# Kernel tuning notes

Hardware: AMD Instinct MI355X
Metric: run time of the kernel (lower is better)

The kernel has to match this reference:

```python
import jax, jax.numpy as jnp
import numpy as np

N, E = 50000, 800000
IN, H, C = 256, 8, 32  # heads=8, hidden_dim=32 -> out dim 256
NEG_SLOPE = 0.2
EPS = 1e-5


def setup_inputs() -> dict:
    key = jax.random.key(0)
    ks = jax.random.split(key, 6)
    x = jax.random.normal(ks[0], (N, IN), jnp.float32)
    edge_index = jax.random.randint(ks[1], (2, E), 0, N, dtype=jnp.int32)
    W = jax.random.normal(ks[2], (IN, H * C), jnp.float32) / np.sqrt(IN).astype(np.float32)
    att_src = jax.random.normal(ks[3], (H, C), jnp.float32) * 0.1
    att_dst = jax.random.normal(ks[4], (H, C), jnp.float32) * 0.1
    bias = jnp.zeros((H * C,), jnp.float32)
    gamma = jnp.ones((H * C,), jnp.float32)
    beta = jnp.zeros((H * C,), jnp.float32)
    return {"x": x, "edge_index": edge_index, "W": W, "att_src": att_src,
            "att_dst": att_dst, "bias": bias, "gamma": gamma, "beta": beta}


def reference(x, edge_index, W, att_src, att_dst, bias, gamma, beta):
    n = x.shape[0]
    # Linear projection -> per-head features [N, H, C]
    xl = (x @ W).reshape(n, H, C)
    # Per-node attention half-logits [N, H]
    a_src = jnp.einsum('nhc,hc->nh', xl, att_src)
    a_dst = jnp.einsum('nhc,hc->nh', xl, att_dst)
    # Add self loops (PyG GATConv default)
    loops = jnp.arange(n, dtype=edge_index.dtype)
    src = jnp.concatenate([edge_index[0], loops])  # [E+N]
    dst = jnp.concatenate([edge_index[1], loops])
    # Edge attention logits + segment softmax over destination neighborhoods
    logits = jax.nn.leaky_relu(a_src[src] + a_dst[dst], NEG_SLOPE)  # [E+N, H]
    seg_max = jax.ops.segment_max(logits, dst, num_segments=n)
    ex = jnp.exp(logits - seg_max[dst])
    denom = jax.ops.segment_sum(ex, dst, num_segments=n)
    alpha = ex / denom[dst]  # [E+N, H]
    # Weighted scatter-aggregation of source features
    msgs = xl[src] * alpha[:, :, None]  # [E+N, H, C]
    out = jax.ops.segment_sum(msgs, dst, num_segments=n).reshape(n, H * C) + bias
    # LayerNorm over feature dim
    mu = jnp.mean(out, axis=-1, keepdims=True)
    var = jnp.var(out, axis=-1, keepdims=True)
    return (out - mu) / jnp.sqrt(var + EPS) * gamma + beta
```

## Files before the change

### kernel.cpp

```cpp
#include <hip/hip_runtime.h>
#include <math.h>

#define NEG 0.2f
#define LNEPS 1e-5f

typedef __attribute__((ext_vector_type(8))) short bf16x8;
typedef __attribute__((ext_vector_type(8))) unsigned short u16x8;
typedef __attribute__((ext_vector_type(4))) float f32x4;
typedef __attribute__((ext_vector_type(4))) unsigned int u32x4;

__device__ __forceinline__ float lrelu(float x){ return x > 0.f ? x : NEG*x; }

__device__ __forceinline__ short f2b(float f){
  unsigned u = __float_as_uint(f);
  unsigned r = u + 0x7fffu + ((u >> 16) & 1u);
  return (short)(r >> 16);
}
__device__ __forceinline__ float b2f(unsigned short u){
  return __uint_as_float(((unsigned)u) << 16);
}
__device__ __forceinline__ unsigned cvtpk(float lo, float hi){
  unsigned r;
  asm("v_cvt_pk_bf16_f32 %0, %1, %2" : "=v"(r) : "v"(lo), "v"(hi));
  return r;
}

__global__ __launch_bounds__(256) void wt_k(const float* __restrict__ W,
                                            const float* __restrict__ att_src,
                                            const float* __restrict__ att_dst,
                                            unsigned short* __restrict__ WT,
                                            unsigned short* __restrict__ WS,
                                            int* __restrict__ deg, int N){
  int b = blockIdx.x;
  if (b < 256){
    int idx = b*256 + threadIdx.x;
    int k = idx >> 8, c = idx & 255;
    WT[c*256 + k] = (unsigned short)f2b(W[idx]);
  } else if (b < 272){
    int idx = (b-256)*256 + threadIdx.x;
    int col = idx >> 8;
    int k   = idx & 255;
    int head = col & 7;
    const float* av = (col < 8 ? att_src : att_dst) + head*32;
    const float* wr = W + (size_t)k*256 + head*32;
    float sum = 0.f;
    #pragma unroll
    for (int c=0;c<32;c++) sum += wr[c]*av[c];
    WS[col*256 + k] = (unsigned short)f2b(sum);
  } else {
    int i = (b-272)*256 + threadIdx.x;
    if (i < N) deg[i] = 1;
  }
}

__device__ __forceinline__ void load_half(float4 nx[8], const float* p){
  #pragma unroll
  for (int s=0;s<4;s++){
    nx[2*s]   = *(const float4*)(p + s*32);
    nx[2*s+1] = *(const float4*)(p + s*32 + 4);
  }
}
__device__ __forceinline__ void cvt_half(bf16x8 af[4], const float4 nx[8]){
  #pragma unroll
  for (int s=0;s<4;s++){
    u32x4 q;
    q.x = cvtpk(nx[2*s].x,   nx[2*s].y);
    q.y = cvtpk(nx[2*s].z,   nx[2*s].w);
    q.z = cvtpk(nx[2*s+1].x, nx[2*s+1].y);
    q.w = cvtpk(nx[2*s+1].z, nx[2*s+1].w);
    af[s] = __builtin_bit_cast(bf16x8, q);
  }
}

__global__ __launch_bounds__(256, 2) void mfma_gemm_k(const float* __restrict__ A,
    const unsigned short* __restrict__ WT, const unsigned short* __restrict__ WS,
    unsigned short* __restrict__ Cb,
    float* __restrict__ a_src, float* __restrict__ a_dst, int M, int nTiles){
  int w   = threadIdx.x >> 6;
  int l   = threadIdx.x & 63;
  int l15 = l & 15;
  int kg  = l >> 4;
  int colbase = w*64;

  bf16x8 bfr[4][8];
  #pragma unroll
  for (int j=0;j<4;j++){
    const unsigned short* bp = WT + (size_t)(colbase + j*16 + l15)*256 + kg*8;
    #pragma unroll
    for (int ks=0;ks<8;ks++) bfr[j][ks] = *(const bf16x8*)(bp + ks*32);
  }
  bf16x8 bfa[8];
  if (w==0){
    const unsigned short* bp = WS + (size_t)l15*256 + kg*8;
    #pragma unroll
    for (int ks=0;ks<8;ks++) bfa[ks] = *(const bf16x8*)(bp + ks*32);
  }

  int t = blockIdx.x;
  if (t >= nTiles) return;
  int row0 = t*16 + l15;
  const float* ap = A + (size_t)(row0 < M ? row0 : M-1)*256 + kg*8;
  float4 nx[8];
  load_half(nx, ap);

  while (t < nTiles){
    f32x4 acc[4];
    #pragma unroll
    for (int j=0;j<4;j++) acc[j] = (f32x4){0.f,0.f,0.f,0.f};
    f32x4 acc_a = (f32x4){0.f,0.f,0.f,0.f};
    bf16x8 af[4];

    cvt_half(af, nx);
    load_half(nx, ap + 128);
    #pragma unroll
    for (int s=0;s<4;s++){
      #pragma unroll
      for (int j=0;j<4;j++)
        acc[j] = __builtin_amdgcn_mfma_f32_16x16x32_bf16(af[s], bfr[j][s], acc[j], 0, 0, 0);
      if (w==0)
        acc_a = __builtin_amdgcn_mfma_f32_16x16x32_bf16(af[s], bfa[s], acc_a, 0, 0, 0);
    }

    int tn = t + gridDim.x;
    int rown = tn < nTiles ? tn*16 + l15 : row0;
    const float* apn = A + (size_t)(rown < M ? rown : M-1)*256 + kg*8;

    cvt_half(af, nx);
    load_half(nx, apn);
    #pragma unroll
    for (int s=0;s<4;s++){
      #pragma unroll
      for (int j=0;j<4;j++)
        acc[j] = __builtin_amdgcn_mfma_f32_16x16x32_bf16(af[s], bfr[j][4+s], acc[j], 0, 0, 0);
      if (w==0)
        acc_a = __builtin_amdgcn_mfma_f32_16x16x32_bf16(af[s], bfa[4+s], acc_a, 0, 0, 0);
    }

    int orow_base = t*16 + kg*4;
    #pragma unroll
    for (int j=0;j<4;j++){
      #pragma unroll
      for (int rp=0;rp<2;rp++){
        unsigned pk = cvtpk(acc[j][2*rp], acc[j][2*rp+1]);
        int orow = orow_base + 2*rp;
        if (orow < M)   Cb[(size_t)orow*256     + colbase + j*16 + l15] = (unsigned short)(pk & 0xffffu);
        if (orow+1 < M) Cb[(size_t)(orow+1)*256 + colbase + j*16 + l15] = (unsigned short)(pk >> 16);
      }
    }
    if (w==0){
      #pragma unroll
      for (int rr=0;rr<4;rr++){
        int orow = orow_base + rr;
        if (orow < M){
          if (l15 < 8) a_src[(size_t)orow*8 + l15]     = acc_a[rr];
          else         a_dst[(size_t)orow*8 + l15 - 8] = acc_a[rr];
        }
      }
    }
    t = tn; row0 = rown; ap = apn;
  }
}

__global__ void deg_k(const int* __restrict__ dst, int* __restrict__ deg, int E){
  int e = blockIdx.x*blockDim.x+threadIdx.x;
  if (e<E) atomicAdd(&deg[dst[e]],1);
}

__global__ __launch_bounds__(1024) void scan1_k(const int* __restrict__ deg,
                                                int* __restrict__ off,
                                                int* __restrict__ bsum, int n){
  __shared__ int wsum[16];
  int tid=threadIdx.x, lane=tid&63, wid=tid>>6;
  int i = blockIdx.x*1024 + tid;
  int v = (i<n)?deg[i]:0;
  int x = v;
  #pragma unroll
  for (int s=1;s<64;s<<=1){ int t2=__shfl_up(x,s); if (lane>=s) x+=t2; }
  if (lane==63) wsum[wid]=x;
  __syncthreads();
  if (tid<16){
    int y=wsum[tid];
    #pragma unroll
    for (int s=1;s<16;s<<=1){ int t2=__shfl_up(y,s); if (tid>=s) y+=t2; }
    wsum[tid]=y;
  }
  __syncthreads();
  int prefix=(wid? wsum[wid-1]:0);
  if (i<n) off[i]=prefix + x - v;
  if (tid==0) bsum[blockIdx.x]=wsum[15];
}

__global__ void scan2_k(int* __restrict__ bsum, int nb, int* __restrict__ offn){
  int lane = threadIdx.x;
  int v = (lane<nb)?bsum[lane]:0;
  int x = v;
  #pragma unroll
  for (int s=1;s<64;s<<=1){ int t2=__shfl_up(x,s); if (lane>=s) x+=t2; }
  if (lane<nb) bsum[lane] = x - v;
  if (lane==63) *offn = x;
}

__global__ __launch_bounds__(1024) void scan3self_k(int* __restrict__ off,
    const int* __restrict__ bsum, int* __restrict__ sorted, int* __restrict__ cur, int n){
  int i = blockIdx.x*1024 + threadIdx.x;
  if (i>=n) return;
  int o = off[i] + bsum[blockIdx.x];
  off[i] = o;
  sorted[o] = i;
  cur[i] = 1;
}

__global__ void scatter_k(const int* __restrict__ src, const int* __restrict__ dst,
                          const int* __restrict__ off, int* __restrict__ cur,
                          int* __restrict__ sorted, int E){
  int e=blockIdx.x*blockDim.x+threadIdx.x;
  if (e<E){
    int d=dst[e];
    int pos=off[d]+atomicAdd(&cur[d],1);
    sorted[pos]=src[e];
  }
}

__global__ __launch_bounds__(256) void agg5_k(const unsigned short* __restrict__ xlb,
    const float* __restrict__ a_src, const float* __restrict__ a_dst,
    const int* __restrict__ off, const int* __restrict__ sorted,
    const float* __restrict__ bias, const float* __restrict__ gamma,
    const float* __restrict__ beta, float* __restrict__ out, int n){
  int node = blockIdx.x*4 + (threadIdx.x>>6);
  if (node >= n) return;
  int lane = threadIdx.x & 63;
  int half = lane >> 5;
  int sl   = lane & 31;
  int h    = sl >> 2;
  int hh   = lane & 7;
  int je   = lane >> 3;
  float adst_h = a_dst[(size_t)node*8 + h];
  float adst_e = a_dst[(size_t)node*8 + hh];
  int s0 = off[node], dd = off[node+1] - s0;

  float acc[8] = {0.f,0.f,0.f,0.f,0.f,0.f,0.f,0.f};
  float den = 0.f;

  int i = 0;
  for (; i+8 <= dd; i += 8){
    int s[4];
    #pragma unroll
    for (int j=0;j<4;j++) s[j] = sorted[s0 + i + 2*j + half];
    int se = sorted[s0 + i + je];
    float w_l = __expf(lrelu(a_src[(size_t)se*8 + hh] + adst_e));
    float wv[4];
    #pragma unroll
    for (int j=0;j<4;j++) wv[j] = __shfl(w_l, ((2*j+half)<<3) | h);
    u16x8 u[4];
    #pragma unroll
    for (int j=0;j<4;j++) u[j] = *(const u16x8*)(xlb + (size_t)s[j]*256 + sl*8);
    #pragma unroll
    for (int j=0;j<4;j++){
      den += wv[j];
      #pragma unroll
      for (int k=0;k<8;k++) acc[k] += wv[j]*b2f((unsigned short)u[j][k]);
    }
  }
  for (; i < dd; i += 2){
    int idx = i + half;
    bool ok = idx < dd;
    int s1 = ok ? sorted[s0+idx] : node;
    float w1 = ok ? __expf(lrelu(a_src[(size_t)s1*8+h]+adst_h)) : 0.f;
    u16x8 u1 = *(const u16x8*)(xlb + (size_t)s1*256 + sl*8);
    den += w1;
    #pragma unroll
    for (int k=0;k<8;k++) acc[k] += w1*b2f((unsigned short)u1[k]);
  }

  den += __shfl_xor(den, 32);
  #pragma unroll
  for (int k=0;k<8;k++) acc[k] += __shfl_xor(acc[k], 32);

  float rd = 1.0f/den;
  float4 bia0 = *(const float4*)(bias + sl*8);
  float4 bia1 = *(const float4*)(bias + sl*8 + 4);
  float o[8];
  o[0]=acc[0]*rd+bia0.x; o[1]=acc[1]*rd+bia0.y; o[2]=acc[2]*rd+bia0.z; o[3]=acc[3]*rd+bia0.w;
  o[4]=acc[4]*rd+bia1.x; o[5]=acc[5]*rd+bia1.y; o[6]=acc[6]*rd+bia1.z; o[7]=acc[7]*rd+bia1.w;

  float sum=0.f, ssq=0.f;
  #pragma unroll
  for (int k=0;k<8;k++){ sum += o[k]; ssq += o[k]*o[k]; }
  #pragma unroll
  for (int s=1;s<32;s<<=1){ sum += __shfl_xor(sum,s); ssq += __shfl_xor(ssq,s); }
  float mean = sum*(1.0f/256.0f);
  float var  = ssq*(1.0f/256.0f) - mean*mean;
  float rstd = rsqrtf(var + LNEPS);

  int f = sl*8 + half*4;
  float4 g  = *(const float4*)(gamma + f);
  float4 be = *(const float4*)(beta + f);
  int kb = half*4;
  float4 ov;
  ov.x = (o[kb+0]-mean)*rstd*g.x+be.x;
  ov.y = (o[kb+1]-mean)*rstd*g.y+be.y;
  ov.z = (o[kb+2]-mean)*rstd*g.z+be.z;
  ov.w = (o[kb+3]-mean)*rstd*g.w+be.w;
  *(float4*)(out + (size_t)node*256 + f) = ov;
}

extern "C" void kernel_launch(void* const* d_in, const int* in_sizes, int n_in,
                              void* d_out, int out_size, void* d_ws, size_t ws_size,
                              hipStream_t stream){
  const float* x       = (const float*)d_in[0];
  const int*   ei      = (const int*)  d_in[1];
  const float* W       = (const float*)d_in[2];
  const float* att_src = (const float*)d_in[3];
  const float* att_dst = (const float*)d_in[4];
  const float* bias    = (const float*)d_in[5];
  const float* gamma   = (const float*)d_in[6];
  const float* beta    = (const float*)d_in[7];
  float* out = (float*)d_out;

  int N = in_sizes[0]/256;
  int E = in_sizes[1]/2;
  const int* srcp = ei;
  const int* dstp = ei + E;

  unsigned short* xlb = (unsigned short*)d_ws;
  float* a_src = (float*)(xlb + (size_t)N*256);
  float* a_dst = a_src + (size_t)N*8;
  int*   deg   = (int*)(a_dst + (size_t)N*8);
  int*   off   = deg + N;
  int*   cur   = off + N + 1;
  int*   sorted= cur + N;
  int*   bsum  = sorted + E + N;
  unsigned short* WT = (unsigned short*)(bsum + 1024);
  unsigned short* WS = WT + 65536;

  int nb = (N + 1023)/1024;
  int nbI = (N + 255)/256;
  int nTiles = (N + 15)/16;

  wt_k<<<272 + nbI, 256, 0, stream>>>(W, att_src, att_dst, WT, WS, deg, N);
  mfma_gemm_k<<<512, 256, 0, stream>>>(x, WT, WS, xlb, a_src, a_dst, N, nTiles);
  deg_k<<<(E+255)/256, 256, 0, stream>>>(dstp, deg, E);
  scan1_k<<<nb, 1024, 0, stream>>>(deg, off, bsum, N);
  scan2_k<<<1, 64, 0, stream>>>(bsum, nb, off + N);
  scan3self_k<<<nb, 1024, 0, stream>>>(off, bsum, sorted, cur, N);
  scatter_k<<<(E+255)/256, 256, 0, stream>>>(srcp, dstp, off, cur, sorted, E);
  agg5_k<<<(N+3)/4, 256, 0, stream>>>(xlb, a_src, a_dst, off, sorted, bias, gamma, beta, out, N);
}
```

Baseline: 210.8 us.

## Stage GEMM A tile through swizzled LDS and merge degree/scan launches

```diff
diff --git a/kernel.cpp b/kernel.cpp
--- a/kernel.cpp
+++ b/kernel.cpp
@@ -28,9 +28,10 @@
 __global__ __launch_bounds__(256) void wt_k(const float* __restrict__ W,
                                             const float* __restrict__ att_src,
                                             const float* __restrict__ att_dst,
+                                            const int* __restrict__ dst,
                                             unsigned short* __restrict__ WT,
                                             unsigned short* __restrict__ WS,
-                                            int* __restrict__ deg, int N){
+                                            int* __restrict__ deg, int E){
   int b = blockIdx.x;
   if (b < 256){
     int idx = b*256 + threadIdx.x;
@@ -45,30 +46,24 @@
     const float* wr = W + (size_t)k*256 + head*32;
     float sum = 0.f;
     #pragma unroll
-    for (int c=0;c<32;c++) sum += wr[c]*av[c];
+    for (int c2=0;c2<32;c2++) sum += wr[c2]*av[c2];
     WS[col*256 + k] = (unsigned short)f2b(sum);
   } else {
-    int i = (b-272)*256 + threadIdx.x;
-    if (i < N) deg[i] = 1;
-  }
-}
-
-__device__ __forceinline__ void load_half(float4 nx[8], const float* p){
-  #pragma unroll
-  for (int s=0;s<4;s++){
-    nx[2*s]   = *(const float4*)(p + s*32);
-    nx[2*s+1] = *(const float4*)(p + s*32 + 4);
-  }
-}
-__device__ __forceinline__ void cvt_half(bf16x8 af[4], const float4 nx[8]){
-  #pragma unroll
-  for (int s=0;s<4;s++){
-    u32x4 q;
-    q.x = cvtpk(nx[2*s].x,   nx[2*s].y);
-    q.y = cvtpk(nx[2*s].z,   nx[2*s].w);
-    q.z = cvtpk(nx[2*s+1].x, nx[2*s+1].y);
-    q.w = cvtpk(nx[2*s+1].z, nx[2*s+1].w);
-    af[s] = __builtin_bit_cast(bf16x8, q);
+    int e = (b-272)*256 + threadIdx.x;
+    if (e < E) atomicAdd(&deg[dst[e]], 1);
+  }
+}
+
+__device__ __forceinline__ void load_tile(float4 v[4], const float* __restrict__ A,
+                                          int t, int M, int tid){
+  const float* base = A + (size_t)t*4096;
+  int rmax = M - 1 - t*16;
+  #pragma unroll
+  for (int j=0;j<4;j++){
+    int idx4 = (j>>1)*512 + 2*tid + (j&1);
+    int r = idx4 >> 6;
+    if (r > rmax) idx4 = (rmax<<6) | (idx4 & 63);
+    v[j] = *(const float4*)(base + (size_t)idx4*4);
   }
 }
 
@@ -76,8 +71,10 @@
     const unsigned short* __restrict__ WT, const unsigned short* __restrict__ WS,
     unsigned short* __restrict__ Cb,
     float* __restrict__ a_src, float* __restrict__ a_dst, int M, int nTiles){
-  int w   = threadIdx.x >> 6;
-  int l   = threadIdx.x & 63;
+  __shared__ __align__(16) unsigned short Asb[16*256];
+  int tid = threadIdx.x;
+  int w   = tid >> 6;
+  int l   = tid & 63;
   int l15 = l & 15;
   int kg  = l >> 4;
   int colbase = w*64;
@@ -98,42 +95,42 @@
 
   int t = blockIdx.x;
   if (t >= nTiles) return;
-  int row0 = t*16 + l15;
-  const float* ap = A + (size_t)(row0 < M ? row0 : M-1)*256 + kg*8;
-  float4 nx[8];
-  load_half(nx, ap);
+  float4 v[4];
+  load_tile(v, A, t, M, tid);
 
   while (t < nTiles){
+    __syncthreads();
+    #pragma unroll
+    for (int p=0;p<2;p++){
+      u32x4 q;
+      q.x = cvtpk(v[2*p].x,   v[2*p].y);
+      q.y = cvtpk(v[2*p].z,   v[2*p].w);
+      q.z = cvtpk(v[2*p+1].x, v[2*p+1].y);
+      q.w = cvtpk(v[2*p+1].z, v[2*p+1].w);
+      int slot = p*256 + tid;
+      int sw = slot ^ ((slot>>5)&7);
+      *(u32x4*)(Asb + (size_t)sw*8) = q;
+    }
+    __syncthreads();
+
+    int tn = t + gridDim.x;
+    if (tn < nTiles) load_tile(v, A, tn, M, tid);
+
     f32x4 acc[4];
     #pragma unroll
     for (int j=0;j<4;j++) acc[j] = (f32x4){0.f,0.f,0.f,0.f};
     f32x4 acc_a = (f32x4){0.f,0.f,0.f,0.f};
-    bf16x8 af[4];
-
-    cvt_half(af, nx);
-    load_half(nx, ap + 128);
-    #pragma unroll
-    for (int s=0;s<4;s++){
+
+    #pragma unroll
+    for (int s=0;s<8;s++){
+      int slot = l15*32 + kg + s*4;
+      int sw = slot ^ (l15 & 7);
+      bf16x8 af = *(const bf16x8*)(Asb + (size_t)sw*8);
       #pragma unroll
       for (int j=0;j<4;j++)
-        acc[j] = __builtin_amdgcn_mfma_f32_16x16x32_bf16(af[s], bfr[j][s], acc[j], 0, 0, 0);
+        acc[j] = __builtin_amdgcn_mfma_f32_16x16x32_bf16(af, bfr[j][s], acc[j], 0, 0, 0);
       if (w==0)
-        acc_a = __builtin_amdgcn_mfma_f32_16x16x32_bf16(af[s], bfa[s], acc_a, 0, 0, 0);
-    }
-
-    int tn = t + gridDim.x;
-    int rown = tn < nTiles ? tn*16 + l15 : row0;
-    const float* apn = A + (size_t)(rown < M ? rown : M-1)*256 + kg*8;
-
-    cvt_half(af, nx);
-    load_half(nx, apn);
-    #pragma unroll
-    for (int s=0;s<4;s++){
-      #pragma unroll
-      for (int j=0;j<4;j++)
-        acc[j] = __builtin_amdgcn_mfma_f32_16x16x32_bf16(af[s], bfr[j][4+s], acc[j], 0, 0, 0);
-      if (w==0)
-        acc_a = __builtin_amdgcn_mfma_f32_16x16x32_bf16(af[s], bfa[4+s], acc_a, 0, 0, 0);
+        acc_a = __builtin_amdgcn_mfma_f32_16x16x32_bf16(af, bfa[s], acc_a, 0, 0, 0);
     }
 
     int orow_base = t*16 + kg*4;
@@ -157,13 +154,8 @@
         }
       }
     }
-    t = tn; row0 = rown; ap = apn;
-  }
-}
-
-__global__ void deg_k(const int* __restrict__ dst, int* __restrict__ deg, int E){
-  int e = blockIdx.x*blockDim.x+threadIdx.x;
-  if (e<E) atomicAdd(&deg[dst[e]],1);
+    t = tn;
+  }
 }
 
 __global__ __launch_bounds__(1024) void scan1_k(const int* __restrict__ deg,
@@ -172,7 +164,7 @@
   __shared__ int wsum[16];
   int tid=threadIdx.x, lane=tid&63, wid=tid>>6;
   int i = blockIdx.x*1024 + tid;
-  int v = (i<n)?deg[i]:0;
+  int v = (i<n)?(deg[i]+1):0;
   int x = v;
   #pragma unroll
   for (int s=1;s<64;s<<=1){ int t2=__shfl_up(x,s); if (lane>=s) x+=t2; }
@@ -190,21 +182,21 @@
   if (tid==0) bsum[blockIdx.x]=wsum[15];
 }
 
-__global__ void scan2_k(int* __restrict__ bsum, int nb, int* __restrict__ offn){
-  int lane = threadIdx.x;
-  int v = (lane<nb)?bsum[lane]:0;
-  int x = v;
-  #pragma unroll
-  for (int s=1;s<64;s<<=1){ int t2=__shfl_up(x,s); if (lane>=s) x+=t2; }
-  if (lane<nb) bsum[lane] = x - v;
-  if (lane==63) *offn = x;
-}
-
 __global__ __launch_bounds__(1024) void scan3self_k(int* __restrict__ off,
-    const int* __restrict__ bsum, int* __restrict__ sorted, int* __restrict__ cur, int n){
+    const int* __restrict__ bsum, int* __restrict__ sorted, int* __restrict__ cur,
+    int n, int total){
+  __shared__ int prefs;
+  if (threadIdx.x < 64){
+    int v = ((int)threadIdx.x < blockIdx.x) ? bsum[threadIdx.x] : 0;
+    #pragma unroll
+    for (int s=1;s<64;s<<=1) v += __shfl_xor(v, s);
+    if (threadIdx.x==0) prefs = v;
+  }
+  __syncthreads();
   int i = blockIdx.x*1024 + threadIdx.x;
+  if (blockIdx.x==0 && threadIdx.x==0) off[n] = total;
   if (i>=n) return;
-  int o = off[i] + bsum[blockIdx.x];
+  int o = off[i] + prefs;
   off[i] = o;
   sorted[o] = i;
   cur[i] = 1;
@@ -334,15 +326,13 @@
   unsigned short* WS = WT + 65536;
 
   int nb = (N + 1023)/1024;
-  int nbI = (N + 255)/256;
   int nTiles = (N + 15)/16;
 
-  wt_k<<<272 + nbI, 256, 0, stream>>>(W, att_src, att_dst, WT, WS, deg, N);
+  hipMemsetAsync(deg, 0, (size_t)N*sizeof(int), stream);
+  wt_k<<<272 + (E+255)/256, 256, 0, stream>>>(W, att_src, att_dst, dstp, WT, WS, deg, E);
   mfma_gemm_k<<<512, 256, 0, stream>>>(x, WT, WS, xlb, a_src, a_dst, N, nTiles);
-  deg_k<<<(E+255)/256, 256, 0, stream>>>(dstp, deg, E);
   scan1_k<<<nb, 1024, 0, stream>>>(deg, off, bsum, N);
-  scan2_k<<<1, 64, 0, stream>>>(bsum, nb, off + N);
-  scan3self_k<<<nb, 1024, 0, stream>>>(off, bsum, sorted, cur, N);
+  scan3self_k<<<nb, 1024, 0, stream>>>(off, bsum, sorted, cur, N, E + N);
   scatter_k<<<(E+255)/256, 256, 0, stream>>>(srcp, dstp, off, cur, sorted, E);
   agg5_k<<<(N+3)/4, 256, 0, stream>>>(xlb, a_src, a_dst, off, sorted, bias, gamma, beta, out, N);
 }
```

New measurement: 193.9 us. 8.0% less time.
